# Kernel tuning notes

Measured on AMD Instinct MI355X. Metric: run time of the kernel, lower is better.

The kernel has to match this reference:

```python
import jax, jax.numpy as jnp
import numpy as np

B, N, D, K, CF = 2, 4096, 128, 32, 16
EI = 2 * D + 1  # edge_input_dim = 257 (edge_feat=0, fourier_feat=0)


def setup_inputs() -> dict:
    key = jax.random.key(0)
    ks = jax.random.split(key, 10)
    rn = lambda k, shp, s=0.05: jax.random.normal(k, shp, jnp.float32) * s
    return {
        "h": rn(ks[0], (B, N, D), 1.0),
        "x": rn(ks[1], (B, N, 3), 1.0),
        "mask": jnp.ones((B, N), dtype=bool),
        # edge_mlp: Linear(EI, 2EI) -> SiLU -> Linear(2EI, CF) -> SiLU
        "We1": rn(ks[2], (EI, 2 * EI)), "be1": jnp.zeros((2 * EI,), jnp.float32),
        "We2": rn(ks[3], (2 * EI, CF)), "be2": jnp.zeros((CF,), jnp.float32),
        # coors_mlp: Linear(CF, 4CF) -> SiLU -> Linear(4CF, 1)
        "Wc1": rn(ks[4], (CF, 4 * CF)), "bc1": jnp.zeros((4 * CF,), jnp.float32),
        "Wc2": rn(ks[5], (4 * CF, 1)), "bc2": jnp.zeros((1,), jnp.float32),
        # node_mlp: Linear(D+CF, 2D) -> SiLU -> Linear(2D, D)
        "Wn1": rn(ks[6], (D + CF, 2 * D)), "bn1": jnp.zeros((2 * D,), jnp.float32),
        "Wn2": rn(ks[7], (2 * D, D)), "bn2": jnp.zeros((D,), jnp.float32),
    }


def _forward(h, x, mask, We1, be1, We2, be2, Wc1, bc1, Wc2, bc2, Wn1, bn1, Wn2, bn2):
    silu = jax.nn.silu
    b, n, d = h.shape
    # pairwise relative coordinates and squared distances
    rel = x[:, :, None, :] - x[:, None, :, :]            # [b, n, n, 3]
    dist = jnp.sum(rel * rel, axis=-1)                   # [b, n, n]
    # top-K nearest neighbors (smallest distance)
    _, idx = jax.lax.top_k(-dist, K)                     # [b, n, K]
    rel_k = jnp.take_along_axis(rel, idx[..., None], axis=2)   # [b, n, K, 3]
    dist_k = jnp.take_along_axis(dist, idx, axis=2)[..., None]  # [b, n, K, 1]
    bidx = jnp.arange(b)[:, None, None]
    feats_j = h[bidx, idx]                               # [b, n, K, d]
    feats_i = jnp.broadcast_to(h[:, :, None, :], (b, n, K, d))
    edge_in = jnp.concatenate([feats_i, feats_j, dist_k], axis=-1)  # [b, n, K, 2d+1]
    # edge MLP
    m_ij = silu(silu(edge_in @ We1 + be1) @ We2 + be2)   # [b, n, K, CF]
    # coordinate weights
    cw = (silu(m_ij @ Wc1 + bc1) @ Wc2 + bc2)[..., 0]    # [b, n, K]
    mask_ij = mask[:, :, None] & mask[bidx, idx]         # [b, n, K]
    cw = jnp.where(mask_ij, cw, 0.0)
    coors_out = jnp.einsum('bij,bijc->bic', cw, rel_k) + x
    # node update
    m_i = m_ij.sum(axis=-2)                              # [b, n, CF]
    node_in = jnp.concatenate([h, m_i], axis=-1)
    node_out = silu(node_in @ Wn1 + bn1) @ Wn2 + bn2 + h
    return node_out, coors_out


def reference(h, x, mask, We1, be1, We2, be2, Wc1, bc1, Wc2, bc2, Wn1, bn1, Wn2, bn2):
    return _forward(h, x, mask, We1, be1, We2, be2, Wc1, bc1, Wc2, bc2, Wn1, bn1, Wn2, bn2)
```

## Files before the change

### kernel.cpp

```cpp
#include <hip/hip_runtime.h>
#include <hip/hip_bf16.h>

#define BB    2
#define NNODE 4096
#define DD    128
#define KK    32
#define CFX   16

typedef __attribute__((ext_vector_type(8))) short bf16x8;
typedef __attribute__((ext_vector_type(4))) float f32x4;

__device__ __forceinline__ unsigned short f2bf(float f) {
    __hip_bfloat16 h = __float2bfloat16(f);
    return *reinterpret_cast<unsigned short*>(&h);
}
__device__ __forceinline__ unsigned pk2(float lo, float hi) {
    __hip_bfloat162 v = __float22bfloat162_rn(make_float2(lo, hi));
    return *reinterpret_cast<unsigned*>(&v);
}
__device__ __forceinline__ float silu_f(float v) {
    float e = __expf(-v);
    return v * __builtin_amdgcn_rcpf(1.f + e);
}
__device__ __forceinline__ float dist3(float xi0, float xi1, float xi2,
                                       const float* __restrict__ xb, int j) {
    float d0 = __fsub_rn(xi0, xb[3 * j]);
    float d1 = __fsub_rn(xi1, xb[3 * j + 1]);
    float d2 = __fsub_rn(xi2, xb[3 * j + 2]);
    return __fadd_rn(__fadd_rn(__fmul_rn(d0, d0), __fmul_rn(d1, d1)), __fmul_rn(d2, d2));
}

__global__ void prep_kernel(const float* __restrict__ We1, const float* __restrict__ We2,
                            const float* __restrict__ Wn1, const float* __restrict__ Wn2,
                            unsigned short* __restrict__ W1pack, unsigned short* __restrict__ W2p2,
                            unsigned short* __restrict__ Wn1p, unsigned short* __restrict__ Wn2p) {
    int tid = blockIdx.x * 256 + threadIdx.x;
    int stride = gridDim.x * 256;
    for (int p = tid; p < 9 * 36 * 64 * 8; p += stride) {
        int i = p & 7, lane = (p >> 3) & 63, rest = p >> 9;
        int nb = rest % 36, ks = rest / 36;
        int n = nb * 16 + (lane & 15);
        int k = ks * 32 + 8 * (lane >> 4) + i;
        W1pack[p] = (k < 257 && n < 514) ? f2bf(We1[k * 514 + n]) : (unsigned short)0;
    }
    for (int p = tid; p < 4 * 5 * 64 * 8; p += stride) {
        int i = p & 7, lane = (p >> 3) & 63, rest = p >> 9;
        int ks2 = rest % 5, wn = rest / 5;
        int g = lane >> 4, f = lane & 15;
        int nloc = ks2 * 32 + 16 * (i >> 2) + 4 * g + (i & 3);
        int ng = wn * 144 + nloc;
        W2p2[p] = (nloc < 144 && ng < 514) ? f2bf(We2[ng * 16 + f]) : (unsigned short)0;
    }
    for (int p = tid; p < 5 * 16 * 64 * 8; p += stride) {
        int i = p & 7, lane = (p >> 3) & 63, rest = p >> 9;
        int nb = rest % 16, ks = rest / 16;
        int u = nb * 16 + (lane & 15);
        int k = ks * 32 + 8 * (lane >> 4) + i;
        Wn1p[p] = (k < 144) ? f2bf(Wn1[k * 256 + u]) : (unsigned short)0;
    }
    for (int p = tid; p < 8 * 8 * 64 * 8; p += stride) {
        int i = p & 7, lane = (p >> 3) & 63, rest = p >> 9;
        int nb = rest % 8, ks = rest / 8;
        int d = nb * 16 + (lane & 15);
        int k = ks * 32 + 8 * (lane >> 4) + i;
        Wn2p[p] = f2bf(Wn2[k * 128 + d]);
    }
}

__global__ __launch_bounds__(256) void pre_kernel(
    const float* __restrict__ h, const float* __restrict__ be1,
    const unsigned short* __restrict__ W1pack,
    float* __restrict__ preI_g, unsigned short* __restrict__ preJ_g)
{
    __shared__ unsigned short nin[16][136];
    const int t = threadIdx.x;
    const int gn0 = blockIdx.x * 16;
    const int wn = t >> 6, lane = t & 63;
    const int l15 = lane & 15, g = lane >> 4;

    for (int q = t; q < 16 * 32; q += 256) {
        int node = q >> 5, c4 = q & 31;
        float4 v = *(const float4*)(h + (size_t)(gn0 + node) * DD + c4 * 4);
        *(uint2*)&nin[node][c4 * 4] = make_uint2(pk2(v.x, v.y), pk2(v.z, v.w));
    }
    __syncthreads();

    const bf16x8* W1v = (const bf16x8*)W1pack;
    {
        f32x4 acc[9];
        #pragma unroll
        for (int nb = 0; nb < 9; ++nb)
            #pragma unroll
            for (int r = 0; r < 4; ++r) acc[nb][r] = 0.f;
        #pragma unroll
        for (int ks = 0; ks < 4; ++ks) {
            bf16x8 bfr = *(const bf16x8*)&nin[l15][ks * 32 + 8 * g];
            #pragma unroll
            for (int nb = 0; nb < 9; ++nb) {
                bf16x8 af = W1v[((size_t)(ks * 36 + wn * 9 + nb)) * 64 + lane];
                acc[nb] = __builtin_amdgcn_mfma_f32_16x16x32_bf16(af, bfr, acc[nb], 0, 0, 0);
            }
        }
        float* outp = preI_g + (size_t)(gn0 + l15) * 576;
        #pragma unroll
        for (int nb = 0; nb < 9; ++nb) {
            int n0 = wn * 144 + nb * 16 + 4 * g;
            float4 o;
            o.x = acc[nb][0] + ((n0 + 0) < 514 ? be1[n0 + 0] : 0.f);
            o.y = acc[nb][1] + ((n0 + 1) < 514 ? be1[n0 + 1] : 0.f);
            o.z = acc[nb][2] + ((n0 + 2) < 514 ? be1[n0 + 2] : 0.f);
            o.w = acc[nb][3] + ((n0 + 3) < 514 ? be1[n0 + 3] : 0.f);
            *(float4*)(outp + n0) = o;
        }
    }
    {
        f32x4 acc[9];
        #pragma unroll
        for (int nb = 0; nb < 9; ++nb)
            #pragma unroll
            for (int r = 0; r < 4; ++r) acc[nb][r] = 0.f;
        #pragma unroll
        for (int ks = 0; ks < 4; ++ks) {
            bf16x8 bfr = *(const bf16x8*)&nin[l15][ks * 32 + 8 * g];
            #pragma unroll
            for (int nb = 0; nb < 9; ++nb) {
                bf16x8 af = W1v[((size_t)((ks + 4) * 36 + wn * 9 + nb)) * 64 + lane];
                acc[nb] = __builtin_amdgcn_mfma_f32_16x16x32_bf16(af, bfr, acc[nb], 0, 0, 0);
            }
        }
        unsigned short* outp = preJ_g + (size_t)(gn0 + l15) * 576;
        #pragma unroll
        for (int nb = 0; nb < 9; ++nb) {
            int n0 = wn * 144 + nb * 16 + 4 * g;
            *(uint2*)(outp + n0) = make_uint2(pk2(acc[nb][0], acc[nb][1]), pk2(acc[nb][2], acc[nb][3]));
        }
    }
}

#define EQCAP 36
#define CANDCAP 1024
__global__ __launch_bounds__(256) void knn_kernel(const float* __restrict__ x,
                                                  int* __restrict__ idx_o,
                                                  float* __restrict__ relk_o,
                                                  float* __restrict__ distk_o) {
    __shared__ unsigned hist[4][256];
    __shared__ unsigned wsum[4];
    __shared__ unsigned sel[2];
    __shared__ unsigned shA, shB;
    __shared__ int out_j[KK];
    __shared__ int eqbuf[EQCAP];
    __shared__ uint2 cand[CANDCAP];

    const int t = threadIdx.x;
    const int ln = t & 63, wv = t >> 6;
    const int gn = blockIdx.x;
    const int b = gn >> 12, i = gn & 4095;
    const float* xb = x + (size_t)b * NNODE * 3;
    const float xi0 = xb[3 * i], xi1 = xb[3 * i + 1], xi2 = xb[3 * i + 2];

    #pragma unroll
    for (int q2 = 0; q2 < 4; ++q2) hist[q2][t] = 0;
    __syncthreads();

    unsigned ub[16];
    #pragma unroll
    for (int s = 0; s < 16; ++s) {
        float d = dist3(xi0, xi1, xi2, xb, t + 256 * s);
        ub[s] = __float_as_uint(d);
        atomicAdd(&hist[wv][ub[s] >> 24], 1u);
    }
    __syncthreads();

    int kk = KK;
    {
        unsigned hv = hist[0][t] + hist[1][t] + hist[2][t] + hist[3][t];
        unsigned v = hv;
        #pragma unroll
        for (int off = 1; off < 64; off <<= 1) {
            unsigned o = __shfl_up(v, off, 64);
            if (ln >= off) v += o;
        }
        if (ln == 63) wsum[wv] = v;
        __syncthreads();
        unsigned add = 0;
        #pragma unroll
        for (int w = 0; w < 4; ++w) add += (w < wv) ? wsum[w] : 0u;
        unsigned incl = v + add, excl = incl - hv;
        if ((unsigned)kk > excl && (unsigned)kk <= incl) { sel[0] = (unsigned)t; sel[1] = (unsigned)kk - excl; }
        __syncthreads();
    }
    unsigned prefix = sel[0];
    kk = (int)sel[1];
    __syncthreads();

    unsigned pc = 0;
    #pragma unroll
    for (int s = 0; s < 16; ++s) {
        unsigned tb = ub[s] >> 24;
        pc += (tb < prefix) ? 0x10000u : (tb == prefix ? 1u : 0u);
    }
    {
        unsigned v = pc;
        #pragma unroll
        for (int off = 1; off < 64; off <<= 1) {
            unsigned o = __shfl_up(v, off, 64);
            if (ln >= off) v += o;
        }
        if (ln == 63) wsum[wv] = v;
        __syncthreads();
        unsigned add = 0;
        #pragma unroll
        for (int w = 0; w < 4; ++w) add += (w < wv) ? wsum[w] : 0u;
        unsigned incl = v + add, excl = incl - pc;
        if (t == 255) { shA = incl >> 16; shB = incl & 0xFFFFu; }
        __syncthreads();
        unsigned wl = excl >> 16, wc = excl & 0xFFFFu;
        #pragma unroll
        for (int s = 0; s < 16; ++s) {
            unsigned u = ub[s];
            unsigned tb = u >> 24;
            int j = t + 256 * s;
            if (tb < prefix) { out_j[wl++] = j; }
            else if (tb == prefix) { if (wc < CANDCAP) cand[wc] = make_uint2(u, (unsigned)j); ++wc; }
        }
    }
    __syncthreads();
    const unsigned totL0 = shA, totC = shB;
    const bool fullscan = (totC > CANDCAP);

    for (int r = 1; r < 4; ++r) {
        const int sh = 24 - 8 * r;
        #pragma unroll
        for (int q2 = 0; q2 < 4; ++q2) hist[q2][t] = 0;
        __syncthreads();
        if (!fullscan) {
            for (int ii = t; ii < (int)totC; ii += 256) {
                unsigned u = cand[ii].x;
                if ((u >> (sh + 8)) == prefix) atomicAdd(&hist[wv][(u >> sh) & 255], 1u);
            }
        } else {
            #pragma unroll
            for (int s = 0; s < 16; ++s) {
                unsigned u = ub[s];
                if ((u >> (sh + 8)) == prefix) atomicAdd(&hist[wv][(u >> sh) & 255], 1u);
            }
        }
        __syncthreads();
        unsigned hv = hist[0][t] + hist[1][t] + hist[2][t] + hist[3][t];
        unsigned v = hv;
        #pragma unroll
        for (int off = 1; off < 64; off <<= 1) {
            unsigned o = __shfl_up(v, off, 64);
            if (ln >= off) v += o;
        }
        if (ln == 63) wsum[wv] = v;
        __syncthreads();
        unsigned add = 0;
        #pragma unroll
        for (int w = 0; w < 4; ++w) add += (w < wv) ? wsum[w] : 0u;
        unsigned incl = v + add, excl = incl - hv;
        if ((unsigned)kk > excl && (unsigned)kk <= incl) { sel[0] = (unsigned)t; sel[1] = (unsigned)kk - excl; }
        __syncthreads();
        prefix = (prefix << 8) | sel[0];
        kk = (int)sel[1];
        __syncthreads();
    }
    const unsigned T = prefix;

    int totL;
    if (!fullscan) {
        unsigned pc2 = 0;
        for (int ii = t; ii < (int)totC; ii += 256) {
            unsigned u = cand[ii].x;
            pc2 += (u < T) ? 0x10000u : (u == T ? 1u : 0u);
        }
        unsigned v = pc2;
        #pragma unroll
        for (int off = 1; off < 64; off <<= 1) {
            unsigned o = __shfl_up(v, off, 64);
            if (ln >= off) v += o;
        }
        if (ln == 63) wsum[wv] = v;
        __syncthreads();
        unsigned add = 0;
        #pragma unroll
        for (int w = 0; w < 4; ++w) add += (w < wv) ? wsum[w] : 0u;
        unsigned incl = v + add, excl = incl - pc2;
        if (t == 255) { shA = incl >> 16; shB = incl & 0xFFFFu; }
        __syncthreads();
        unsigned w2 = totL0 + (excl >> 16), we = excl & 0xFFFFu;
        for (int ii = t; ii < (int)totC; ii += 256) {
            unsigned u = cand[ii].x;
            int j = (int)cand[ii].y;
            if (u < T) { out_j[w2++] = j; }
            else if (u == T) { if (we < EQCAP) eqbuf[we] = j; ++we; }
        }
        __syncthreads();
        totL = (int)(totL0 + shA);
        const unsigned totE = shB;
        if (t == 0) {
            int need = KK - totL;
            if (totE <= EQCAP) {
                for (int a = 1; a < (int)totE; ++a) {
                    int key = eqbuf[a], c = a - 1;
                    while (c >= 0 && eqbuf[c] > key) { eqbuf[c + 1] = eqbuf[c]; --c; }
                    eqbuf[c + 1] = key;
                }
                for (int q = 0; q < need; ++q) out_j[totL + q] = eqbuf[q];
            } else {
                int taken = 0;
                for (int j = 0; j < NNODE && taken < need; ++j)
                    if (__float_as_uint(dist3(xi0, xi1, xi2, xb, j)) == T) out_j[totL + taken++] = j;
            }
        }
    } else {
        unsigned pc2 = 0;
        #pragma unroll
        for (int s = 0; s < 16; ++s) {
            unsigned u = ub[s];
            pc2 += (u < T) ? 0x10000u : (u == T ? 1u : 0u);
        }
        unsigned v = pc2;
        #pragma unroll
        for (int off = 1; off < 64; off <<= 1) {
            unsigned o = __shfl_up(v, off, 64);
            if (ln >= off) v += o;
        }
        if (ln == 63) wsum[wv] = v;
        __syncthreads();
        unsigned add = 0;
        #pragma unroll
        for (int w = 0; w < 4; ++w) add += (w < wv) ? wsum[w] : 0u;
        unsigned incl = v + add, excl = incl - pc2;
        if (t == 255) { shA = incl >> 16; shB = incl & 0xFFFFu; }
        __syncthreads();
        unsigned w2 = excl >> 16, we = excl & 0xFFFFu;
        #pragma unroll
        for (int s = 0; s < 16; ++s) {
            unsigned u = ub[s];
            int j = t + 256 * s;
            if (u < T) { out_j[w2++] = j; }
            else if (u == T) { if (we < EQCAP) eqbuf[we] = j; ++we; }
        }
        __syncthreads();
        totL = (int)shA;
        const unsigned totE = shB;
        if (t == 0) {
            int need = KK - totL;
            if (totE <= EQCAP) {
                for (int a = 1; a < (int)totE; ++a) {
                    int key = eqbuf[a], c = a - 1;
                    while (c >= 0 && eqbuf[c] > key) { eqbuf[c + 1] = eqbuf[c]; --c; }
                    eqbuf[c + 1] = key;
                }
                for (int q = 0; q < need; ++q) out_j[totL + q] = eqbuf[q];
            } else {
                int taken = 0;
                for (int j = 0; j < NNODE && taken < need; ++j)
                    if (__float_as_uint(dist3(xi0, xi1, xi2, xb, j)) == T) out_j[totL + taken++] = j;
            }
        }
    }
    __syncthreads();

    if (t < KK) {
        int j = out_j[t];
        size_t eo = (size_t)gn * KK + t;
        idx_o[eo] = j;
        float r0 = __fsub_rn(xi0, xb[3 * j]);
        float r1 = __fsub_rn(xi1, xb[3 * j + 1]);
        float r2 = __fsub_rn(xi2, xb[3 * j + 2]);
        relk_o[eo * 3 + 0] = r0;
        relk_o[eo * 3 + 1] = r1;
        relk_o[eo * 3 + 2] = r2;
        distk_o[eo] = __fadd_rn(__fadd_rn(__fmul_rn(r0, r0), __fmul_rn(r1, r1)), __fmul_rn(r2, r2));
    }
}

__global__ __launch_bounds__(256) void edge_kernel(
    const float* __restrict__ x, const int* __restrict__ mask,
    const float* __restrict__ We1, const float* __restrict__ be2,
    const float* __restrict__ Wc1, const float* __restrict__ bc1,
    const float* __restrict__ Wc2, const float* __restrict__ bc2,
    const int* __restrict__ idx, const float* __restrict__ relk, const float* __restrict__ distk,
    const unsigned short* __restrict__ W2p2,
    const float* __restrict__ preI_g, const unsigned short* __restrict__ preJ_g,
    float* __restrict__ m_i_out, float* __restrict__ coors_out)
{
    __shared__ float pre_s[2 * 576];
    __shared__ float wd_s[576];
    __shared__ int   j_s[64];
    __shared__ float dist_s[64];
    __shared__ float cw_s[64];
    __shared__ float m_s4[4 * 64 * 16];
    __shared__ float m_sF[64 * 17];

    const int t = threadIdx.x;
    const int gn0 = blockIdx.x * 2;
    const int b = gn0 >> 12;
    const int wn = t >> 6, lane = t & 63;
    const int l15 = lane & 15, g = lane >> 4;

    if (t < 64) {
        size_t eo = (size_t)gn0 * KK + t;
        j_s[t] = idx[eo];
        dist_s[t] = distk[eo];
    }
    for (int i2 = t; i2 < 576; i2 += 256) wd_s[i2] = (i2 < 514) ? We1[256 * 514 + i2] : 0.f;
    {
        const float4* src = (const float4*)(preI_g + (size_t)gn0 * 576);
        float4* dst = (float4*)pre_s;
        for (int i2 = t; i2 < 288; i2 += 256) dst[i2] = src[i2];
    }
    __syncthreads();

    const bf16x8* W2v = (const bf16x8*)W2p2;
    int erow[4];
    size_t jrow[4];
    float de[4];
    #pragma unroll
    for (int et = 0; et < 4; ++et) {
        erow[et] = et * 16 + l15;
        jrow[et] = ((size_t)b * NNODE + j_s[erow[et]]) * 576;
        de[et] = dist_s[erow[et]];
    }

    f32x4 acc2[4];
    #pragma unroll
    for (int et = 0; et < 4; ++et)
        #pragma unroll
        for (int r = 0; r < 4; ++r) acc2[et][r] = 0.f;

    #pragma unroll
    for (int c = 0; c < 2; ++c) {
        f32x4 acc[4][4];
        #pragma unroll
        for (int nb = 0; nb < 4; ++nb) {
            const int n0 = wn * 144 + (c * 4 + nb) * 16 + 4 * g;
            f32x4 wdv = *(const f32x4*)&wd_s[n0];
            #pragma unroll
            for (int et = 0; et < 4; ++et) {
                f32x4 pi = *(const f32x4*)&pre_s[(et >> 1) * 576 + n0];
                uint2 pj = *(const uint2*)(preJ_g + jrow[et] + n0);
                float p0 = __uint_as_float(pj.x << 16);
                float p1 = __uint_as_float(pj.x & 0xFFFF0000u);
                float p2 = __uint_as_float(pj.y << 16);
                float p3 = __uint_as_float(pj.y & 0xFFFF0000u);
                acc[nb][et][0] = silu_f(pi[0] + p0 + de[et] * wdv[0]);
                acc[nb][et][1] = silu_f(pi[1] + p1 + de[et] * wdv[1]);
                acc[nb][et][2] = silu_f(pi[2] + p2 + de[et] * wdv[2]);
                acc[nb][et][3] = silu_f(pi[3] + p3 + de[et] * wdv[3]);
            }
        }
        #pragma unroll
        for (int qq = 0; qq < 2; ++qq) {
            int ks2 = 2 * c + qq;
            bf16x8 a2 = W2v[(size_t)(wn * 5 + ks2) * 64 + lane];
            #pragma unroll
            for (int et = 0; et < 4; ++et) {
                union { unsigned u[4]; bf16x8 v; } cv;
                cv.u[0] = pk2(acc[2 * qq][et][0], acc[2 * qq][et][1]);
                cv.u[1] = pk2(acc[2 * qq][et][2], acc[2 * qq][et][3]);
                cv.u[2] = pk2(acc[2 * qq + 1][et][0], acc[2 * qq + 1][et][1]);
                cv.u[3] = pk2(acc[2 * qq + 1][et][2], acc[2 * qq + 1][et][3]);
                acc2[et] = __builtin_amdgcn_mfma_f32_16x16x32_bf16(a2, cv.v, acc2[et], 0, 0, 0);
            }
        }
    }
    {
        f32x4 acc8[4];
        const int n0 = wn * 144 + 128 + 4 * g;
        f32x4 wdv = *(const f32x4*)&wd_s[n0];
        #pragma unroll
        for (int et = 0; et < 4; ++et) {
            f32x4 pi = *(const f32x4*)&pre_s[(et >> 1) * 576 + n0];
            uint2 pj = *(const uint2*)(preJ_g + jrow[et] + n0);
            float p0 = __uint_as_float(pj.x << 16);
            float p1 = __uint_as_float(pj.x & 0xFFFF0000u);
            float p2 = __uint_as_float(pj.y << 16);
            float p3 = __uint_as_float(pj.y & 0xFFFF0000u);
            acc8[et][0] = silu_f(pi[0] + p0 + de[et] * wdv[0]);
            acc8[et][1] = silu_f(pi[1] + p1 + de[et] * wdv[1]);
            acc8[et][2] = silu_f(pi[2] + p2 + de[et] * wdv[2]);
            acc8[et][3] = silu_f(pi[3] + p3 + de[et] * wdv[3]);
        }
        bf16x8 a2 = W2v[(size_t)(wn * 5 + 4) * 64 + lane];
        #pragma unroll
        for (int et = 0; et < 4; ++et) {
            union { unsigned u[4]; bf16x8 v; } cv;
            cv.u[0] = pk2(acc8[et][0], acc8[et][1]);
            cv.u[1] = pk2(acc8[et][2], acc8[et][3]);
            cv.u[2] = 0; cv.u[3] = 0;
            acc2[et] = __builtin_amdgcn_mfma_f32_16x16x32_bf16(a2, cv.v, acc2[et], 0, 0, 0);
        }
    }
    #pragma unroll
    for (int et = 0; et < 4; ++et)
        *(f32x4*)&m_s4[((wn * 64) + erow[et]) * 16 + 4 * g] = acc2[et];
    __syncthreads();

    #pragma unroll
    for (int i2 = t; i2 < 64 * 16; i2 += 256) {
        int e = i2 >> 4, f = i2 & 15;
        float s = m_s4[e * 16 + f] + m_s4[(64 + e) * 16 + f]
                + m_s4[(128 + e) * 16 + f] + m_s4[(192 + e) * 16 + f];
        m_sF[e * 17 + f] = silu_f(s + be2[f]);
    }
    __syncthreads();

    {
        const int ee = t >> 2, q4 = t & 3;
        const int u0 = q4 * 16;
        float mm[16];
        #pragma unroll
        for (int f = 0; f < 16; ++f) mm[f] = m_sF[ee * 17 + f];
        float h2[16];
        {
            const float4* bp = (const float4*)(bc1 + u0);
            float4 b0 = bp[0], b1 = bp[1], b2v = bp[2], b3 = bp[3];
            h2[0]=b0.x; h2[1]=b0.y; h2[2]=b0.z; h2[3]=b0.w;
            h2[4]=b1.x; h2[5]=b1.y; h2[6]=b1.z; h2[7]=b1.w;
            h2[8]=b2v.x; h2[9]=b2v.y; h2[10]=b2v.z; h2[11]=b2v.w;
            h2[12]=b3.x; h2[13]=b3.y; h2[14]=b3.z; h2[15]=b3.w;
        }
        #pragma unroll
        for (int f = 0; f < 16; ++f) {
            const float4* wp = (const float4*)(Wc1 + (size_t)f * 64 + u0);
            float4 w0 = wp[0], w1 = wp[1], w2 = wp[2], w3 = wp[3];
            float v = mm[f];
            h2[0]  = fmaf(v, w0.x, h2[0]);  h2[1]  = fmaf(v, w0.y, h2[1]);
            h2[2]  = fmaf(v, w0.z, h2[2]);  h2[3]  = fmaf(v, w0.w, h2[3]);
            h2[4]  = fmaf(v, w1.x, h2[4]);  h2[5]  = fmaf(v, w1.y, h2[5]);
            h2[6]  = fmaf(v, w1.z, h2[6]);  h2[7]  = fmaf(v, w1.w, h2[7]);
            h2[8]  = fmaf(v, w2.x, h2[8]);  h2[9]  = fmaf(v, w2.y, h2[9]);
            h2[10] = fmaf(v, w2.z, h2[10]); h2[11] = fmaf(v, w2.w, h2[11]);
            h2[12] = fmaf(v, w3.x, h2[12]); h2[13] = fmaf(v, w3.y, h2[13]);
            h2[14] = fmaf(v, w3.z, h2[14]); h2[15] = fmaf(v, w3.w, h2[15]);
        }
        float cw = 0.f;
        const float4* cp = (const float4*)(Wc2 + u0);
        float4 c0 = cp[0], c1 = cp[1], c2 = cp[2], c3 = cp[3];
        const float wv[16] = {c0.x,c0.y,c0.z,c0.w, c1.x,c1.y,c1.z,c1.w,
                              c2.x,c2.y,c2.z,c2.w, c3.x,c3.y,c3.z,c3.w};
        #pragma unroll
        for (int r = 0; r < 16; ++r) cw = fmaf(silu_f(h2[r]), wv[r], cw);
        cw += __shfl_xor(cw, 1, 64);
        cw += __shfl_xor(cw, 2, 64);
        if (q4 == 0) {
            cw += bc2[0];
            int gnode = gn0 + (ee >> 5);
            int mi = mask[gnode];
            int mj = mask[b * NNODE + j_s[ee]];
            cw_s[ee] = (mi != 0 && mj != 0) ? cw : 0.f;
        }
    }
    __syncthreads();

    if (t < 32) {
        int n = t >> 4, f = t & 15;
        float s = 0.f;
        #pragma unroll
        for (int k2 = 0; k2 < 32; ++k2) s += m_sF[(n * 32 + k2) * 17 + f];
        m_i_out[(size_t)(gn0 + n) * CFX + f] = s;
    } else if (t < 38) {
        int r = t - 32;
        int n = r / 3, c = r - n * 3;
        const float* rp = relk + ((size_t)gn0 * KK + n * 32) * 3 + c;
        float s = 0.f;
        #pragma unroll
        for (int k2 = 0; k2 < 32; ++k2) s = fmaf(cw_s[n * 32 + k2], rp[k2 * 3], s);
        coors_out[(size_t)(gn0 + n) * 3 + c] = s + x[(size_t)(gn0 + n) * 3 + c];
    }
}

__global__ __launch_bounds__(256) void node_kernel(
    const float* __restrict__ h, const float* __restrict__ m_i,
    const unsigned short* __restrict__ Wn1p, const float* __restrict__ bn1,
    const unsigned short* __restrict__ Wn2p, const float* __restrict__ bn2,
    float* __restrict__ node_out)
{
    __shared__ unsigned short nin[32][168];
    __shared__ unsigned short hid[32][264];

    const int t = threadIdx.x;
    const int gn0 = blockIdx.x * 32;
    const int wn = t >> 6, lane = t & 63;
    const int l15 = lane & 15, g = lane >> 4;

    for (int q = t; q < 32 * 32; q += 256) {
        int node = q >> 5, c4 = q & 31;
        float4 v = *(const float4*)(h + (size_t)(gn0 + node) * DD + c4 * 4);
        *(uint2*)&nin[node][c4 * 4] = make_uint2(pk2(v.x, v.y), pk2(v.z, v.w));
    }
    if (t < 128) {
        int node = t >> 2, c4 = t & 3;
        float4 v = *(const float4*)(m_i + (size_t)(gn0 + node) * CFX + c4 * 4);
        *(uint2*)&nin[node][128 + c4 * 4] = make_uint2(pk2(v.x, v.y), pk2(v.z, v.w));
    } else if (t < 224) {
        int r = t - 128;
        int node = r / 3, cc = (r - node * 3) * 8;
        *(uint4*)&nin[node][144 + cc] = make_uint4(0, 0, 0, 0);
    }
    __syncthreads();

    const bf16x8* A1 = (const bf16x8*)Wn1p;
    f32x4 acc[4][2];
    #pragma unroll
    for (int nb = 0; nb < 4; ++nb)
        #pragma unroll
        for (int et = 0; et < 2; ++et)
            #pragma unroll
            for (int r = 0; r < 4; ++r) acc[nb][et][r] = 0.f;
    #pragma unroll
    for (int ks = 0; ks < 5; ++ks) {
        const bf16x8* wp = A1 + ((size_t)(ks * 16 + wn * 4)) * 64 + lane;
        bf16x8 afr[4];
        #pragma unroll
        for (int nb = 0; nb < 4; ++nb) afr[nb] = wp[nb * 64];
        bf16x8 b0 = *(const bf16x8*)&nin[l15][ks * 32 + 8 * g];
        bf16x8 b1 = *(const bf16x8*)&nin[16 + l15][ks * 32 + 8 * g];
        #pragma unroll
        for (int nb = 0; nb < 4; ++nb) {
            acc[nb][0] = __builtin_amdgcn_mfma_f32_16x16x32_bf16(afr[nb], b0, acc[nb][0], 0, 0, 0);
            acc[nb][1] = __builtin_amdgcn_mfma_f32_16x16x32_bf16(afr[nb], b1, acc[nb][1], 0, 0, 0);
        }
    }
    #pragma unroll
    for (int nb = 0; nb < 4; ++nb) {
        int u0 = (wn * 4 + nb) * 16 + 4 * g;
        f32x4 bv = *(const f32x4*)&bn1[u0];
        #pragma unroll
        for (int et = 0; et < 2; ++et) {
            float s0 = silu_f(acc[nb][et][0] + bv[0]);
            float s1 = silu_f(acc[nb][et][1] + bv[1]);
            float s2 = silu_f(acc[nb][et][2] + bv[2]);
            float s3 = silu_f(acc[nb][et][3] + bv[3]);
            *(uint2*)&hid[et * 16 + l15][u0] = make_uint2(pk2(s0, s1), pk2(s2, s3));
        }
    }
    __syncthreads();

    const bf16x8* A2 = (const bf16x8*)Wn2p;
    f32x4 acc2[2][2];
    #pragma unroll
    for (int nb = 0; nb < 2; ++nb)
        #pragma unroll
        for (int et = 0; et < 2; ++et)
            #pragma unroll
            for (int r = 0; r < 4; ++r) acc2[nb][et][r] = 0.f;
    #pragma unroll
    for (int ks = 0; ks < 8; ++ks) {
        const bf16x8* wp = A2 + ((size_t)(ks * 8 + wn * 2)) * 64 + lane;
        bf16x8 a0 = wp[0], a1 = wp[64];
        bf16x8 b0 = *(const bf16x8*)&hid[l15][ks * 32 + 8 * g];
        bf16x8 b1 = *(const bf16x8*)&hid[16 + l15][ks * 32 + 8 * g];
        acc2[0][0] = __builtin_amdgcn_mfma_f32_16x16x32_bf16(a0, b0, acc2[0][0], 0, 0, 0);
        acc2[0][1] = __builtin_amdgcn_mfma_f32_16x16x32_bf16(a0, b1, acc2[0][1], 0, 0, 0);
        acc2[1][0] = __builtin_amdgcn_mfma_f32_16x16x32_bf16(a1, b0, acc2[1][0], 0, 0, 0);
        acc2[1][1] = __builtin_amdgcn_mfma_f32_16x16x32_bf16(a1, b1, acc2[1][1], 0, 0, 0);
    }
    #pragma unroll
    for (int nb = 0; nb < 2; ++nb) {
        int d0 = (wn * 2 + nb) * 16 + 4 * g;
        f32x4 bv = *(const f32x4*)&bn2[d0];
        #pragma unroll
        for (int et = 0; et < 2; ++et) {
            int gnode = gn0 + et * 16 + l15;
            float4 hv = *(const float4*)(h + (size_t)gnode * DD + d0);
            float4 o;
            o.x = acc2[nb][et][0] + bv[0] + hv.x;
            o.y = acc2[nb][et][1] + bv[1] + hv.y;
            o.z = acc2[nb][et][2] + bv[2] + hv.z;
            o.w = acc2[nb][et][3] + bv[3] + hv.w;
            *(float4*)(node_out + (size_t)gnode * DD + d0) = o;
        }
    }
}

extern "C" void kernel_launch(void* const* d_in, const int* in_sizes, int n_in,
                              void* d_out, int out_size, void* d_ws, size_t ws_size,
                              hipStream_t stream) {
    const float* h   = (const float*)d_in[0];
    const float* x   = (const float*)d_in[1];
    const int*   mask= (const int*)d_in[2];
    const float* We1 = (const float*)d_in[3];
    const float* be1 = (const float*)d_in[4];
    const float* We2 = (const float*)d_in[5];
    const float* be2 = (const float*)d_in[6];
    const float* Wc1 = (const float*)d_in[7];
    const float* bc1 = (const float*)d_in[8];
    const float* Wc2 = (const float*)d_in[9];
    const float* bc2 = (const float*)d_in[10];
    const float* Wn1 = (const float*)d_in[11];
    const float* bn1 = (const float*)d_in[12];
    const float* Wn2 = (const float*)d_in[13];
    const float* bn2 = (const float*)d_in[14];

    float* node_out  = (float*)d_out;
    float* coors_out = node_out + (size_t)BB * NNODE * DD;

    char* ws = (char*)d_ws;
    int*   idx    = (int*)ws;            ws += (size_t)BB * NNODE * KK * 4;
    float* relk   = (float*)ws;          ws += (size_t)BB * NNODE * KK * 3 * 4;
    float* distk  = (float*)ws;          ws += (size_t)BB * NNODE * KK * 4;
    float* m_i    = (float*)ws;          ws += (size_t)BB * NNODE * CFX * 4;
    unsigned short* W1pack = (unsigned short*)ws;  ws += (size_t)9 * 36 * 64 * 8 * 2;
    unsigned short* W2p2   = (unsigned short*)ws;  ws += (size_t)4 * 5 * 64 * 8 * 2;
    unsigned short* Wn1p   = (unsigned short*)ws;  ws += (size_t)5 * 16 * 64 * 8 * 2;
    unsigned short* Wn2p   = (unsigned short*)ws;  ws += (size_t)8 * 8 * 64 * 8 * 2;
    float* preI_g = (float*)ws;          ws += (size_t)BB * NNODE * 576 * 4;
    unsigned short* preJ_g = (unsigned short*)ws;  ws += (size_t)BB * NNODE * 576 * 2;

    prep_kernel<<<256, 256, 0, stream>>>(We1, We2, Wn1, Wn2, W1pack, W2p2, Wn1p, Wn2p);
    pre_kernel<<<BB * NNODE / 16, 256, 0, stream>>>(h, be1, W1pack, preI_g, preJ_g);
    knn_kernel<<<BB * NNODE, 256, 0, stream>>>(x, idx, relk, distk);
    edge_kernel<<<BB * NNODE / 2, 256, 0, stream>>>(x, mask, We1, be2, Wc1, bc1, Wc2, bc2,
                                                    idx, relk, distk, W2p2, preI_g, preJ_g,
                                                    m_i, coors_out);
    node_kernel<<<BB * NNODE / 32, 256, 0, stream>>>(h, m_i, Wn1p, bn1, Wn2p, bn2, node_out);
}
```

Baseline: 275.1 us.

## Split edge MLP work by edge rows per wave instead of hidden-dim chunks

```diff
diff --git a/kernel.cpp b/kernel.cpp
--- a/kernel.cpp
+++ b/kernel.cpp
@@ -43,13 +43,11 @@
         int k = ks * 32 + 8 * (lane >> 4) + i;
         W1pack[p] = (k < 257 && n < 514) ? f2bf(We1[k * 514 + n]) : (unsigned short)0;
     }
-    for (int p = tid; p < 4 * 5 * 64 * 8; p += stride) {
-        int i = p & 7, lane = (p >> 3) & 63, rest = p >> 9;
-        int ks2 = rest % 5, wn = rest / 5;
+    for (int p = tid; p < 18 * 64 * 8; p += stride) {
+        int i = p & 7, lane = (p >> 3) & 63, ks2 = p >> 9;
         int g = lane >> 4, f = lane & 15;
-        int nloc = ks2 * 32 + 16 * (i >> 2) + 4 * g + (i & 3);
-        int ng = wn * 144 + nloc;
-        W2p2[p] = (nloc < 144 && ng < 514) ? f2bf(We2[ng * 16 + f]) : (unsigned short)0;
+        int ng = ks2 * 32 + 16 * (i >> 2) + 4 * g + (i & 3);
+        W2p2[p] = (ng < 514) ? f2bf(We2[ng * 16 + f]) : (unsigned short)0;
     }
     for (int p = tid; p < 5 * 16 * 64 * 8; p += stride) {
         int i = p & 7, lane = (p >> 3) & 63, rest = p >> 9;
@@ -392,7 +390,6 @@
     __shared__ int   j_s[64];
     __shared__ float dist_s[64];
     __shared__ float cw_s[64];
-    __shared__ float m_s4[4 * 64 * 16];
     __shared__ float m_sF[64 * 17];
 
     const int t = threadIdx.x;
@@ -415,97 +412,44 @@
     __syncthreads();
 
     const bf16x8* W2v = (const bf16x8*)W2p2;
-    int erow[4];
-    size_t jrow[4];
-    float de[4];
-    #pragma unroll
-    for (int et = 0; et < 4; ++et) {
-        erow[et] = et * 16 + l15;
-        jrow[et] = ((size_t)b * NNODE + j_s[erow[et]]) * 576;
-        de[et] = dist_s[erow[et]];
-    }
-
-    f32x4 acc2[4];
-    #pragma unroll
-    for (int et = 0; et < 4; ++et)
-        #pragma unroll
-        for (int r = 0; r < 4; ++r) acc2[et][r] = 0.f;
-
-    #pragma unroll
-    for (int c = 0; c < 2; ++c) {
-        f32x4 acc[4][4];
-        #pragma unroll
-        for (int nb = 0; nb < 4; ++nb) {
-            const int n0 = wn * 144 + (c * 4 + nb) * 16 + 4 * g;
-            f32x4 wdv = *(const f32x4*)&wd_s[n0];
-            #pragma unroll
-            for (int et = 0; et < 4; ++et) {
-                f32x4 pi = *(const f32x4*)&pre_s[(et >> 1) * 576 + n0];
-                uint2 pj = *(const uint2*)(preJ_g + jrow[et] + n0);
-                float p0 = __uint_as_float(pj.x << 16);
-                float p1 = __uint_as_float(pj.x & 0xFFFF0000u);
-                float p2 = __uint_as_float(pj.y << 16);
-                float p3 = __uint_as_float(pj.y & 0xFFFF0000u);
-                acc[nb][et][0] = silu_f(pi[0] + p0 + de[et] * wdv[0]);
-                acc[nb][et][1] = silu_f(pi[1] + p1 + de[et] * wdv[1]);
-                acc[nb][et][2] = silu_f(pi[2] + p2 + de[et] * wdv[2]);
-                acc[nb][et][3] = silu_f(pi[3] + p3 + de[et] * wdv[3]);
-            }
-        }
-        #pragma unroll
-        for (int qq = 0; qq < 2; ++qq) {
-            int ks2 = 2 * c + qq;
-            bf16x8 a2 = W2v[(size_t)(wn * 5 + ks2) * 64 + lane];
-            #pragma unroll
-            for (int et = 0; et < 4; ++et) {
-                union { unsigned u[4]; bf16x8 v; } cv;
-                cv.u[0] = pk2(acc[2 * qq][et][0], acc[2 * qq][et][1]);
-                cv.u[1] = pk2(acc[2 * qq][et][2], acc[2 * qq][et][3]);
-                cv.u[2] = pk2(acc[2 * qq + 1][et][0], acc[2 * qq + 1][et][1]);
-                cv.u[3] = pk2(acc[2 * qq + 1][et][2], acc[2 * qq + 1][et][3]);
-                acc2[et] = __builtin_amdgcn_mfma_f32_16x16x32_bf16(a2, cv.v, acc2[et], 0, 0, 0);
-            }
-        }
-    }
-    {
-        f32x4 acc8[4];
-        const int n0 = wn * 144 + 128 + 4 * g;
-        f32x4 wdv = *(const f32x4*)&wd_s[n0];
-        #pragma unroll
-        for (int et = 0; et < 4; ++et) {
-            f32x4 pi = *(const f32x4*)&pre_s[(et >> 1) * 576 + n0];
-            uint2 pj = *(const uint2*)(preJ_g + jrow[et] + n0);
-            float p0 = __uint_as_float(pj.x << 16);
-            float p1 = __uint_as_float(pj.x & 0xFFFF0000u);
-            float p2 = __uint_as_float(pj.y << 16);
-            float p3 = __uint_as_float(pj.y & 0xFFFF0000u);
-            acc8[et][0] = silu_f(pi[0] + p0 + de[et] * wdv[0]);
-            acc8[et][1] = silu_f(pi[1] + p1 + de[et] * wdv[1]);
-            acc8[et][2] = silu_f(pi[2] + p2 + de[et] * wdv[2]);
-            acc8[et][3] = silu_f(pi[3] + p3 + de[et] * wdv[3]);
-        }
-        bf16x8 a2 = W2v[(size_t)(wn * 5 + 4) * 64 + lane];
-        #pragma unroll
-        for (int et = 0; et < 4; ++et) {
-            union { unsigned u[4]; bf16x8 v; } cv;
-            cv.u[0] = pk2(acc8[et][0], acc8[et][1]);
-            cv.u[1] = pk2(acc8[et][2], acc8[et][3]);
-            cv.u[2] = 0; cv.u[3] = 0;
-            acc2[et] = __builtin_amdgcn_mfma_f32_16x16x32_bf16(a2, cv.v, acc2[et], 0, 0, 0);
-        }
-    }
-    #pragma unroll
-    for (int et = 0; et < 4; ++et)
-        *(f32x4*)&m_s4[((wn * 64) + erow[et]) * 16 + 4 * g] = acc2[et];
-    __syncthreads();
-
-    #pragma unroll
-    for (int i2 = t; i2 < 64 * 16; i2 += 256) {
-        int e = i2 >> 4, f = i2 & 15;
-        float s = m_s4[e * 16 + f] + m_s4[(64 + e) * 16 + f]
-                + m_s4[(128 + e) * 16 + f] + m_s4[(192 + e) * 16 + f];
-        m_sF[e * 17 + f] = silu_f(s + be2[f]);
-    }
+    const int e = wn * 16 + l15;
+    const int node = wn >> 1;
+    const size_t jrow = ((size_t)b * NNODE + j_s[e]) * 576;
+    const float de = dist_s[e];
+
+    f32x4 acc2;
+    #pragma unroll
+    for (int r = 0; r < 4; ++r) acc2[r] = 0.f;
+
+    #pragma unroll
+    for (int ks2 = 0; ks2 < 18; ++ks2) {
+        const int nlo = ks2 * 32 + 4 * g;
+        const int nhi = nlo + 16;
+        f32x4 pil = *(const f32x4*)&pre_s[node * 576 + nlo];
+        f32x4 pih = *(const f32x4*)&pre_s[node * 576 + nhi];
+        f32x4 wdl = *(const f32x4*)&wd_s[nlo];
+        f32x4 wdh = *(const f32x4*)&wd_s[nhi];
+        uint2 pjl = *(const uint2*)(preJ_g + jrow + nlo);
+        uint2 pjh = *(const uint2*)(preJ_g + jrow + nhi);
+        float a0 = silu_f(pil[0] + __uint_as_float(pjl.x << 16)        + de * wdl[0]);
+        float a1 = silu_f(pil[1] + __uint_as_float(pjl.x & 0xFFFF0000u) + de * wdl[1]);
+        float a2v = silu_f(pil[2] + __uint_as_float(pjl.y << 16)        + de * wdl[2]);
+        float a3 = silu_f(pil[3] + __uint_as_float(pjl.y & 0xFFFF0000u) + de * wdl[3]);
+        float b0 = silu_f(pih[0] + __uint_as_float(pjh.x << 16)        + de * wdh[0]);
+        float b1 = silu_f(pih[1] + __uint_as_float(pjh.x & 0xFFFF0000u) + de * wdh[1]);
+        float b2 = silu_f(pih[2] + __uint_as_float(pjh.y << 16)        + de * wdh[2]);
+        float b3 = silu_f(pih[3] + __uint_as_float(pjh.y & 0xFFFF0000u) + de * wdh[3]);
+        union { unsigned u[4]; bf16x8 v; } cv;
+        cv.u[0] = pk2(a0, a1);
+        cv.u[1] = pk2(a2v, a3);
+        cv.u[2] = pk2(b0, b1);
+        cv.u[3] = pk2(b2, b3);
+        bf16x8 a2f = W2v[(size_t)ks2 * 64 + lane];
+        acc2 = __builtin_amdgcn_mfma_f32_16x16x32_bf16(a2f, cv.v, acc2, 0, 0, 0);
+    }
+    #pragma unroll
+    for (int r = 0; r < 4; ++r)
+        m_sF[e * 17 + 4 * g + r] = silu_f(acc2[r] + be2[4 * g + r]);
     __syncthreads();
 
     {
@@ -705,7 +649,7 @@
     float* distk  = (float*)ws;          ws += (size_t)BB * NNODE * KK * 4;
     float* m_i    = (float*)ws;          ws += (size_t)BB * NNODE * CFX * 4;
     unsigned short* W1pack = (unsigned short*)ws;  ws += (size_t)9 * 36 * 64 * 8 * 2;
-    unsigned short* W2p2   = (unsigned short*)ws;  ws += (size_t)4 * 5 * 64 * 8 * 2;
+    unsigned short* W2p2   = (unsigned short*)ws;  ws += (size_t)18 * 64 * 8 * 2;
     unsigned short* Wn1p   = (unsigned short*)ws;  ws += (size_t)5 * 16 * 64 * 8 * 2;
     unsigned short* Wn2p   = (unsigned short*)ws;  ws += (size_t)8 * 8 * 64 * 8 * 2;
     float* preI_g = (float*)ws;          ws += (size_t)BB * NNODE * 576 * 4;
```

Result: no change. 278.7 us (+1.3%).
